# Performance work log

Measured on AMD Instinct MI355X. Metric: run time of the kernel, lower is better.

The kernel has to match this reference:

```python
import jax, jax.numpy as jnp
import numpy as np

SEQ, B, D_IN, D_TRAJ, D_LSTM = 640, 40, 8, 32, 64
NH, DH = 4, 48  # n_head, att_out
EMB = NH * DH  # 192


def setup_inputs() -> dict:
    key = jax.random.key(0)
    ks = jax.random.split(key, 16)
    g = lambda k, shape: (jax.random.normal(k, shape, dtype=jnp.float32) * 0.05)
    z = lambda n: jnp.zeros((n,), jnp.float32)
    return {
        "hist": jax.random.normal(ks[0], (128, 5, 40, D_IN), dtype=jnp.float32),
        "adj": jnp.zeros((B, B), dtype=jnp.int32),  # unused (use_spatial=False)
        "W1": g(ks[1], (D_TRAJ, D_IN)), "b1": z(D_TRAJ),
        "W_ih": g(ks[2], (4 * D_LSTM, D_TRAJ)), "W_hh": g(ks[3], (4 * D_LSTM, D_LSTM)),
        "b_ih": z(4 * D_LSTM), "b_hh": z(4 * D_LSTM),
        "Wq": g(ks[4], (EMB, D_LSTM)), "bq": z(EMB),
        "Wk": g(ks[5], (EMB, D_LSTM)), "bk": z(EMB),
        "Wv": g(ks[6], (EMB, D_LSTM)), "bv": z(EMB),
        "Wa": g(ks[7], (D_LSTM, EMB)), "ba": z(D_LSTM),
        "Wg": g(ks[8], (D_LSTM, EMB)), "bg": z(D_LSTM),
        "gamma": jnp.ones((D_LSTM,), jnp.float32), "beta": z(D_LSTM),
    }


def reference(hist, adj, W1, b1, W_ih, W_hh, b_ih, b_hh,
              Wq, bq, Wk, bk, Wv, bv, Wa, ba, Wg, bg, gamma, beta):
    # trajectory embedding + ELU
    x = jax.nn.elu(jnp.einsum('...f,hf->...h', hist, W1) + b1)
    x = x.reshape(SEQ, B, D_TRAJ)  # hardcoded (128*5, 40, 32) in the module

    # single-layer LSTM (torch gate order i, f, g, o), seq-first
    def step(carry, xt):
        h, c = carry
        gates = xt @ W_ih.T + h @ W_hh.T + b_ih + b_hh
        i, f, g_, o = jnp.split(gates, 4, axis=-1)
        c = jax.nn.sigmoid(f) * c + jax.nn.sigmoid(i) * jnp.tanh(g_)
        h = jax.nn.sigmoid(o) * jnp.tanh(c)
        return (h, c), h

    h0 = jnp.zeros((B, D_LSTM), x.dtype)
    (_, _), seq = jax.lax.scan(step, (h0, h0), x)  # (640, 40, 64)

    # multi-head attention over the 40-agent axis, per time step
    def heads(W, b):
        y = seq @ W.T + b  # (640, 40, 192)
        return y.reshape(SEQ, B, NH, DH).transpose(2, 0, 1, 3)  # (4, 640, 40, 48)

    q, k, v = heads(Wq, bq), heads(Wk, bk), heads(Wv, bv)
    a = jax.nn.softmax(jnp.einsum('hnqd,hnkd->hnqk', q, k) / 8.0, axis=-1)  # /sqrt(64)
    o = jnp.einsum('hnqk,hnkd->hnqd', a, v)  # (4, 640, 40, 48)
    o = o.transpose(1, 2, 0, 3).reshape(SEQ, B, EMB)  # recombine heads -> (640, 40, 192)

    # GLU (dropout rate = 0)
    tv = (o @ Wa.T + ba) * jax.nn.sigmoid(o @ Wg.T + bg)  # (640, 40, 64)

    # Add & LayerNorm (residual with LSTM output)
    y = seq + tv
    mu = y.mean(-1, keepdims=True)
    var = ((y - mu) ** 2).mean(-1, keepdims=True)
    return (y - mu) / jnp.sqrt(var + 1e-5) * gamma + beta
```

## Files before the change

kernel.cpp:

```cpp
#include <hip/hip_runtime.h>

#define SEQ 640
#define BATCH 40
#define D_IN 8
#define D_TRAJ 32
#define D_LSTM 64
#define G4 256
#define NH 4
#define DH 48
#define EMB 192

typedef float v2f __attribute__((ext_vector_type(2)));
typedef float v4f __attribute__((ext_vector_type(4)));
typedef _Float16 h2t __attribute__((ext_vector_type(2)));

__device__ __forceinline__ float sigmoid_f(float x) {
    float e = __expf(-x);
    return __builtin_amdgcn_rcpf(1.f + e);
}
__device__ __forceinline__ float tanh_f(float x) {
    float e = __expf(2.f * x);
    return 1.f - 2.f * __builtin_amdgcn_rcpf(e + 1.f);
}

__global__ void __launch_bounds__(256) k_embed(
    const float* __restrict__ hist, const float* __restrict__ W1,
    const float* __restrict__ b1, const float* __restrict__ W_ih,
    const float* __restrict__ b_ih, const float* __restrict__ b_hh,
    float* __restrict__ gates_x)
{
    __shared__ float sh_hist[BATCH * D_IN];
    __shared__ float sh_traj[BATCH * D_TRAJ];
    const int t = blockIdx.x, tid = threadIdx.x;

    for (int i = tid; i < BATCH * D_IN; i += 256)
        sh_hist[i] = hist[t * BATCH * D_IN + i];
    __syncthreads();

    for (int idx = tid; idx < BATCH * D_TRAJ; idx += 256) {
        int b = idx >> 5, h = idx & 31;
        float acc = b1[h];
        #pragma unroll
        for (int f = 0; f < D_IN; ++f)
            acc += sh_hist[b * D_IN + f] * W1[h * D_IN + f];
        sh_traj[idx] = acc > 0.f ? acc : (__expf(acc) - 1.f);
    }
    __syncthreads();

    float w[D_TRAJ];
    {
        const v4f* wv = (const v4f*)(W_ih + tid * D_TRAJ);
        #pragma unroll
        for (int u = 0; u < 8; ++u) {
            v4f x = wv[u];
            w[4*u] = x.x; w[4*u+1] = x.y; w[4*u+2] = x.z; w[4*u+3] = x.w;
        }
    }
    const float bias = b_ih[tid] + b_hh[tid];
    const int j = tid & 63, g = tid >> 6;

    for (int b = 0; b < BATCH; ++b) {
        float acc = bias;
        #pragma unroll
        for (int h = 0; h < D_TRAJ; ++h)
            acc += sh_traj[b * D_TRAJ + h] * w[h];
        gates_x[((size_t)b * SEQ + t) * G4 + j * 4 + g] = acc;
    }
}

__global__ void __launch_bounds__(64, 1) k_lstm(
    const float* __restrict__ gates_x, const float* __restrict__ W_hh,
    float* __restrict__ seq_out)
{
    const int b = blockIdx.x, j = threadIdx.x;

    h2t wi2[32], wf2[32], wg2[32], wo2[32];
    const float* Wi = W_hh + (0 * 64 + j) * D_LSTM;
    const float* Wf = W_hh + (1 * 64 + j) * D_LSTM;
    const float* Wg = W_hh + (2 * 64 + j) * D_LSTM;
    const float* Wo = W_hh + (3 * 64 + j) * D_LSTM;
    #pragma unroll
    for (int m = 0; m < 32; ++m) {
        wi2[m] = (h2t){(_Float16)Wi[2 * m], (_Float16)Wi[2 * m + 1]};
        wf2[m] = (h2t){(_Float16)Wf[2 * m], (_Float16)Wf[2 * m + 1]};
        wg2[m] = (h2t){(_Float16)Wg[2 * m], (_Float16)Wg[2 * m + 1]};
        wo2[m] = (h2t){(_Float16)Wo[2 * m], (_Float16)Wo[2 * m + 1]};
    }

    const v4f* gxp = (const v4f*)(gates_x + (size_t)b * SEQ * G4);
    v4f g0 = gxp[0 * 64 + j];
    v4f g1 = gxp[1 * 64 + j];
    v4f g2 = gxp[2 * 64 + j];
    v4f g3 = gxp[3 * 64 + j];

    float h = 0.f, c = 0.f;
    float hpf = 0.f;
    const bool odd = (j & 1);

    auto lstm_step = [&](v4f& gk, int t) {
        const int hbits = __builtin_bit_cast(int, hpf);

        float ai0 = gk.x, af0 = gk.y, ag0 = gk.z, ao0 = gk.w;
        float ai1 = 0.f, af1 = 0.f, ag1 = 0.f, ao1 = 0.f;
        #pragma unroll
        for (int m = 0; m < 16; ++m) {
            int pmi = __builtin_amdgcn_readlane(hbits, 2 * m);
            h2t p = __builtin_bit_cast(h2t, pmi);
            ai0 = __builtin_amdgcn_fdot2(wi2[m], p, ai0, false);
            af0 = __builtin_amdgcn_fdot2(wf2[m], p, af0, false);
            ag0 = __builtin_amdgcn_fdot2(wg2[m], p, ag0, false);
            ao0 = __builtin_amdgcn_fdot2(wo2[m], p, ao0, false);
        }
        #pragma unroll
        for (int m = 16; m < 32; ++m) {
            int pmi = __builtin_amdgcn_readlane(hbits, 2 * m);
            h2t p = __builtin_bit_cast(h2t, pmi);
            ai1 = __builtin_amdgcn_fdot2(wi2[m], p, ai1, false);
            af1 = __builtin_amdgcn_fdot2(wf2[m], p, af1, false);
            ag1 = __builtin_amdgcn_fdot2(wg2[m], p, ag1, false);
            ao1 = __builtin_amdgcn_fdot2(wo2[m], p, ao1, false);
        }
        float ai = ai0 + ai1, af = af0 + af1, ag = ag0 + ag1, ao = ao0 + ao1;

        c = sigmoid_f(af) * c + sigmoid_f(ai) * tanh_f(ag);
        h = sigmoid_f(ao) * tanh_f(c);
        seq_out[(size_t)(t * BATCH + b) * D_LSTM + j] = h;

        int own = (int)__builtin_bit_cast(unsigned short, (_Float16)h);
        int nb  = __builtin_amdgcn_update_dpp(0, own, 0xB1, 0xF, 0xF, true);
        int pk  = odd ? (nb | (own << 16)) : (own | (nb << 16));
        hpf = __builtin_bit_cast(float, pk);

        int tp = t + 4; if (tp > SEQ - 1) tp = SEQ - 1;
        gk = gxp[(size_t)tp * 64 + j];
    };

    for (int t = 0; t < SEQ; t += 4) {
        lstm_step(g0, t + 0);
        lstm_step(g1, t + 1);
        lstm_step(g2, t + 2);
        lstm_step(g3, t + 3);
    }
}

#define SAS 68
#define SKVS 152
#define SSS 44
__global__ void __launch_bounds__(256) k_attn(
    const float* __restrict__ seq,
    const float* __restrict__ Wq, const float* __restrict__ bq,
    const float* __restrict__ Wk, const float* __restrict__ bk,
    const float* __restrict__ Wv, const float* __restrict__ bv,
    float* __restrict__ o_buf)
{
    const int h = blockIdx.x, t = blockIdx.y, tid = threadIdx.x;
    __shared__ float sA[BATCH * SAS];
    __shared__ _Float16 skqv[BATCH * SKVS];
    __shared__ float ss[BATCH * SSS];

    for (int i = tid; i < BATCH * D_LSTM; i += 256)
        sA[(i >> 6) * SAS + (i & 63)] = seq[(size_t)t * BATCH * D_LSTM + i];
    __syncthreads();

    if (tid < 144) {
        int m = tid / 48, d = tid - m * 48;
        const float* W = (m == 0) ? Wq : (m == 1) ? Wk : Wv;
        const float* B = (m == 0) ? bq : (m == 1) ? bk : bv;
        const float* wrow = W + (h * DH + d) * D_LSTM;
        float wreg[D_LSTM];
        {
            const v4f* wv = (const v4f*)wrow;
            #pragma unroll
            for (int u = 0; u < 16; ++u) {
                v4f x = wv[u];
                wreg[4*u] = x.x; wreg[4*u+1] = x.y;
                wreg[4*u+2] = x.z; wreg[4*u+3] = x.w;
            }
        }
        const float bias = B[h * DH + d];

        for (int a = 0; a < BATCH; ++a) {
            const v4f* ap = (const v4f*)&sA[a * SAS];
            float acc = bias;
            #pragma unroll
            for (int u = 0; u < 16; ++u) {
                v4f av = ap[u];
                acc += av.x * wreg[4*u]   + av.y * wreg[4*u+1]
                     + av.z * wreg[4*u+2] + av.w * wreg[4*u+3];
            }
            skqv[a * SKVS + tid] = (_Float16)acc;
        }
    }
    __syncthreads();

    for (int idx = tid; idx < BATCH * BATCH; idx += 256) {
        int i = idx / BATCH, jj = idx % BATCH;
        const v4f* qp = (const v4f*)&skqv[i * SKVS];
        const v4f* kp = (const v4f*)&skqv[jj * SKVS + 48];
        float acc = 0.f;
        #pragma unroll
        for (int u = 0; u < 6; ++u) {
            v4f qv = qp[u], kv = kp[u];
            acc = __builtin_amdgcn_fdot2(__builtin_bit_cast(h2t, qv.x),
                    __builtin_bit_cast(h2t, kv.x), acc, false);
            acc = __builtin_amdgcn_fdot2(__builtin_bit_cast(h2t, qv.y),
                    __builtin_bit_cast(h2t, kv.y), acc, false);
            acc = __builtin_amdgcn_fdot2(__builtin_bit_cast(h2t, qv.z),
                    __builtin_bit_cast(h2t, kv.z), acc, false);
            acc = __builtin_amdgcn_fdot2(__builtin_bit_cast(h2t, qv.w),
                    __builtin_bit_cast(h2t, kv.w), acc, false);
        }
        ss[i * SSS + jj] = acc * 0.125f;
    }
    __syncthreads();

    if (tid < BATCH) {
        v4f* rp = (v4f*)&ss[tid * SSS];
        v4f r[10];
        #pragma unroll
        for (int u = 0; u < 10; ++u) r[u] = rp[u];
        float m = -1e30f;
        #pragma unroll
        for (int u = 0; u < 10; ++u)
            m = fmaxf(m, fmaxf(fmaxf(r[u].x, r[u].y), fmaxf(r[u].z, r[u].w)));
        float s = 0.f;
        #pragma unroll
        for (int u = 0; u < 10; ++u) {
            r[u].x = __expf(r[u].x - m); s += r[u].x;
            r[u].y = __expf(r[u].y - m); s += r[u].y;
            r[u].z = __expf(r[u].z - m); s += r[u].z;
            r[u].w = __expf(r[u].w - m); s += r[u].w;
        }
        float inv = __builtin_amdgcn_rcpf(s);
        #pragma unroll
        for (int u = 0; u < 10; ++u) {
            r[u].x *= inv; r[u].y *= inv; r[u].z *= inv; r[u].w *= inv;
            rp[u] = r[u];
        }
    }
    __syncthreads();

    if (tid < 240) {
        int bi = tid / 6, dg = tid % 6, d0 = dg * 8;
        const v4f* sp = (const v4f*)&ss[bi * SSS];
        v4f sr[10];
        #pragma unroll
        for (int u = 0; u < 10; ++u) sr[u] = sp[u];
        float acc[8];
        #pragma unroll
        for (int d = 0; d < 8; ++d) acc[d] = 0.f;
        for (int jj = 0; jj < 40; ++jj) {
            float a = ((const float*)&sr[jj >> 2])[jj & 3];
            v4f vv = *(const v4f*)&skqv[jj * SKVS + 96 + d0];
            #pragma unroll
            for (int w = 0; w < 4; ++w) {
                h2t pr = __builtin_bit_cast(h2t, ((const float*)&vv)[w]);
                acc[2 * w]     += a * (float)pr[0];
                acc[2 * w + 1] += a * (float)pr[1];
            }
        }
        float* ob = &o_buf[((size_t)t * BATCH + bi) * EMB + h * DH + d0];
        *(v4f*)&ob[0] = (v4f){acc[0], acc[1], acc[2], acc[3]};
        *(v4f*)&ob[4] = (v4f){acc[4], acc[5], acc[6], acc[7]};
    }
}

__global__ void __launch_bounds__(256) k_glu_ln(
    const float* __restrict__ seq, const float* __restrict__ obuf,
    const float* __restrict__ Wa, const float* __restrict__ ba,
    const float* __restrict__ Wg, const float* __restrict__ bg,
    const float* __restrict__ gamma, const float* __restrict__ beta,
    float* __restrict__ out)
{
    const int t = blockIdx.x, tid = threadIdx.x;
    __shared__ float so[BATCH * 193];
    __shared__ float sy[BATCH * 65];
    __shared__ float sseq[BATCH * D_LSTM];

    const float* ot = obuf + (size_t)t * BATCH * EMB;
    for (int i = tid; i < BATCH * EMB; i += 256)
        so[(i / EMB) * 193 + (i % EMB)] = ot[i];
    for (int i = tid; i < BATCH * D_LSTM; i += 256)
        sseq[i] = seq[(size_t)t * BATCH * D_LSTM + i];
    __syncthreads();

    const int j = tid >> 2, bgr = tid & 3;
    float acc_a[10], acc_g[10];
    #pragma unroll
    for (int bb = 0; bb < 10; ++bb) { acc_a[bb] = ba[j]; acc_g[bb] = bg[j]; }

    const float* wa = Wa + j * EMB;
    const float* wg = Wg + j * EMB;
    for (int p = 0; p < EMB; ++p) {
        float a = wa[p], g = wg[p];
        #pragma unroll
        for (int bb = 0; bb < 10; ++bb) {
            float o = so[(bgr + 4 * bb) * 193 + p];
            acc_a[bb] += o * a;
            acc_g[bb] += o * g;
        }
    }
    #pragma unroll
    for (int bb = 0; bb < 10; ++bb) {
        int b = bgr + 4 * bb;
        float tv = acc_a[bb] * sigmoid_f(acc_g[bb]);
        sy[b * 65 + j] = sseq[b * D_LSTM + j] + tv;
    }
    __syncthreads();

    const int w = tid >> 6, lane = tid & 63;
    const float gm = gamma[lane], bt = beta[lane];
    for (int rr = 0; rr < 10; ++rr) {
        int b = w + 4 * rr;
        float y = sy[b * 65 + lane];
        float s1 = y, s2 = y * y;
        #pragma unroll
        for (int m = 1; m < 64; m <<= 1) {
            s1 += __shfl_xor(s1, m, 64);
            s2 += __shfl_xor(s2, m, 64);
        }
        float mu  = s1 * (1.f / 64.f);
        float var = s2 * (1.f / 64.f) - mu * mu;
        float inv = rsqrtf(var + 1e-5f);
        out[(size_t)t * BATCH * D_LSTM + b * D_LSTM + lane] =
            (y - mu) * inv * gm + bt;
    }
}

extern "C" void kernel_launch(void* const* d_in, const int* in_sizes, int n_in,
                              void* d_out, int out_size, void* d_ws, size_t ws_size,
                              hipStream_t stream)
{
    const float* hist = (const float*)d_in[0];
    const float* W1   = (const float*)d_in[2];
    const float* b1   = (const float*)d_in[3];
    const float* W_ih = (const float*)d_in[4];
    const float* W_hh = (const float*)d_in[5];
    const float* b_ih = (const float*)d_in[6];
    const float* b_hh = (const float*)d_in[7];
    const float* Wq   = (const float*)d_in[8];
    const float* bq   = (const float*)d_in[9];
    const float* Wk   = (const float*)d_in[10];
    const float* bk   = (const float*)d_in[11];
    const float* Wv   = (const float*)d_in[12];
    const float* bv   = (const float*)d_in[13];
    const float* Wa   = (const float*)d_in[14];
    const float* ba   = (const float*)d_in[15];
    const float* Wg   = (const float*)d_in[16];
    const float* bg   = (const float*)d_in[17];
    const float* gamma = (const float*)d_in[18];
    const float* beta  = (const float*)d_in[19];
    float* out = (float*)d_out;

    float* ws = (float*)d_ws;
    float* gates_x = ws;
    float* seq     = ws + 6553600;
    float* obuf    = ws + 6553600 + 1638400;

    hipLaunchKernelGGL(k_embed, dim3(SEQ), dim3(256), 0, stream,
                       hist, W1, b1, W_ih, b_ih, b_hh, gates_x);
    hipLaunchKernelGGL(k_lstm, dim3(BATCH), dim3(64), 0, stream,
                       gates_x, W_hh, seq);
    hipLaunchKernelGGL(k_attn, dim3(NH, SEQ), dim3(256), 0, stream,
                       seq, Wq, bq, Wk, bk, Wv, bv, obuf);
    hipLaunchKernelGGL(k_glu_ln, dim3(SEQ), dim3(256), 0, stream,
                       seq, obuf, Wa, ba, Wg, bg, gamma, beta, out);
}
```

Baseline: 496.6 us.

## Split LSTM gates across four wavefronts with LDS exchange per step

The recurrent LSTM kernel now uses 256 threads per batch element, one wavefront per gate, so each lane holds one gate row of W_hh and does 32 dot2 ops per step instead of 128. Gate results are exchanged through a double-buffered shared array with a block barrier every time step. The gates_x layout written by the embedding kernel changes to gate-major so each wave reads its own gate contiguously. This shortens the serial dependency chain per step but adds a barrier and LDS round trip to every one of the 640 steps, and all four waves redundantly compute the cell update.

```diff
diff --git a/kernel.cpp b/kernel.cpp
--- a/kernel.cpp
+++ b/kernel.cpp
@@ -64,67 +64,77 @@
         #pragma unroll
         for (int h = 0; h < D_TRAJ; ++h)
             acc += sh_traj[b * D_TRAJ + h] * w[h];
-        gates_x[((size_t)b * SEQ + t) * G4 + j * 4 + g] = acc;
-    }
-}
-
-__global__ void __launch_bounds__(64, 1) k_lstm(
+        gates_x[(((size_t)b * 4 + g) * SEQ + t) * 64 + j] = acc;
+    }
+}
+
+__global__ void __launch_bounds__(256, 1) k_lstm(
     const float* __restrict__ gates_x, const float* __restrict__ W_hh,
     float* __restrict__ seq_out)
 {
-    const int b = blockIdx.x, j = threadIdx.x;
-
-    h2t wi2[32], wf2[32], wg2[32], wo2[32];
-    const float* Wi = W_hh + (0 * 64 + j) * D_LSTM;
-    const float* Wf = W_hh + (1 * 64 + j) * D_LSTM;
-    const float* Wg = W_hh + (2 * 64 + j) * D_LSTM;
-    const float* Wo = W_hh + (3 * 64 + j) * D_LSTM;
-    #pragma unroll
-    for (int m = 0; m < 32; ++m) {
-        wi2[m] = (h2t){(_Float16)Wi[2 * m], (_Float16)Wi[2 * m + 1]};
-        wf2[m] = (h2t){(_Float16)Wf[2 * m], (_Float16)Wf[2 * m + 1]};
-        wg2[m] = (h2t){(_Float16)Wg[2 * m], (_Float16)Wg[2 * m + 1]};
-        wo2[m] = (h2t){(_Float16)Wo[2 * m], (_Float16)Wo[2 * m + 1]};
-    }
-
-    const v4f* gxp = (const v4f*)(gates_x + (size_t)b * SEQ * G4);
-    v4f g0 = gxp[0 * 64 + j];
-    v4f g1 = gxp[1 * 64 + j];
-    v4f g2 = gxp[2 * 64 + j];
-    v4f g3 = gxp[3 * 64 + j];
+    const int b = blockIdx.x;
+    const int tid = threadIdx.x;
+    const int g = tid >> 6;
+    const int j = tid & 63;
+
+    __shared__ float sg[2][4][64];
+
+    h2t w2[32];
+    {
+        const float* Wrow = W_hh + (g * 64 + j) * D_LSTM;
+        #pragma unroll
+        for (int m = 0; m < 32; ++m)
+            w2[m] = (h2t){(_Float16)Wrow[2*m], (_Float16)Wrow[2*m+1]};
+    }
+
+    const float* gx = gates_x + (((size_t)b * 4 + g) * SEQ) * 64 + j;
+    float gq0 = gx[0 * 64];
+    float gq1 = gx[1 * 64];
+    float gq2 = gx[2 * 64];
+    float gq3 = gx[3 * 64];
 
     float h = 0.f, c = 0.f;
     float hpf = 0.f;
     const bool odd = (j & 1);
 
-    auto lstm_step = [&](v4f& gk, int t) {
+    auto step = [&](float& gq, int t) {
         const int hbits = __builtin_bit_cast(int, hpf);
 
-        float ai0 = gk.x, af0 = gk.y, ag0 = gk.z, ao0 = gk.w;
-        float ai1 = 0.f, af1 = 0.f, ag1 = 0.f, ao1 = 0.f;
-        #pragma unroll
-        for (int m = 0; m < 16; ++m) {
-            int pmi = __builtin_amdgcn_readlane(hbits, 2 * m);
-            h2t p = __builtin_bit_cast(h2t, pmi);
-            ai0 = __builtin_amdgcn_fdot2(wi2[m], p, ai0, false);
-            af0 = __builtin_amdgcn_fdot2(wf2[m], p, af0, false);
-            ag0 = __builtin_amdgcn_fdot2(wg2[m], p, ag0, false);
-            ao0 = __builtin_amdgcn_fdot2(wo2[m], p, ao0, false);
-        }
-        #pragma unroll
-        for (int m = 16; m < 32; ++m) {
-            int pmi = __builtin_amdgcn_readlane(hbits, 2 * m);
-            h2t p = __builtin_bit_cast(h2t, pmi);
-            ai1 = __builtin_amdgcn_fdot2(wi2[m], p, ai1, false);
-            af1 = __builtin_amdgcn_fdot2(wf2[m], p, af1, false);
-            ag1 = __builtin_amdgcn_fdot2(wg2[m], p, ag1, false);
-            ao1 = __builtin_amdgcn_fdot2(wo2[m], p, ao1, false);
-        }
-        float ai = ai0 + ai1, af = af0 + af1, ag = ag0 + ag1, ao = ao0 + ao1;
+        float a0 = gq, a1 = 0.f, a2 = 0.f, a3 = 0.f;
+        #pragma unroll
+        for (int m = 0; m < 8; ++m) {
+            h2t p = __builtin_bit_cast(h2t, __builtin_amdgcn_readlane(hbits, 2*m));
+            a0 = __builtin_amdgcn_fdot2(w2[m], p, a0, false);
+        }
+        #pragma unroll
+        for (int m = 8; m < 16; ++m) {
+            h2t p = __builtin_bit_cast(h2t, __builtin_amdgcn_readlane(hbits, 2*m));
+            a1 = __builtin_amdgcn_fdot2(w2[m], p, a1, false);
+        }
+        #pragma unroll
+        for (int m = 16; m < 24; ++m) {
+            h2t p = __builtin_bit_cast(h2t, __builtin_amdgcn_readlane(hbits, 2*m));
+            a2 = __builtin_amdgcn_fdot2(w2[m], p, a2, false);
+        }
+        #pragma unroll
+        for (int m = 24; m < 32; ++m) {
+            h2t p = __builtin_bit_cast(h2t, __builtin_amdgcn_readlane(hbits, 2*m));
+            a3 = __builtin_amdgcn_fdot2(w2[m], p, a3, false);
+        }
+        float a = (a0 + a1) + (a2 + a3);
+
+        const int buf = t & 1;
+        sg[buf][g][j] = a;
+        __syncthreads();
+        float ai = sg[buf][0][j];
+        float af = sg[buf][1][j];
+        float ag = sg[buf][2][j];
+        float ao = sg[buf][3][j];
 
         c = sigmoid_f(af) * c + sigmoid_f(ai) * tanh_f(ag);
         h = sigmoid_f(ao) * tanh_f(c);
-        seq_out[(size_t)(t * BATCH + b) * D_LSTM + j] = h;
+        if (g == 0)
+            seq_out[(size_t)(t * BATCH + b) * D_LSTM + j] = h;
 
         int own = (int)__builtin_bit_cast(unsigned short, (_Float16)h);
         int nb  = __builtin_amdgcn_update_dpp(0, own, 0xB1, 0xF, 0xF, true);
@@ -132,14 +142,14 @@
         hpf = __builtin_bit_cast(float, pk);
 
         int tp = t + 4; if (tp > SEQ - 1) tp = SEQ - 1;
-        gk = gxp[(size_t)tp * 64 + j];
+        gq = gx[(size_t)tp * 64];
     };
 
     for (int t = 0; t < SEQ; t += 4) {
-        lstm_step(g0, t + 0);
-        lstm_step(g1, t + 1);
-        lstm_step(g2, t + 2);
-        lstm_step(g3, t + 3);
+        step(gq0, t + 0);
+        step(gq1, t + 1);
+        step(gq2, t + 2);
+        step(gq3, t + 3);
     }
 }
 
@@ -359,7 +369,7 @@
 
     hipLaunchKernelGGL(k_embed, dim3(SEQ), dim3(256), 0, stream,
                        hist, W1, b1, W_ih, b_ih, b_hh, gates_x);
-    hipLaunchKernelGGL(k_lstm, dim3(BATCH), dim3(64), 0, stream,
+    hipLaunchKernelGGL(k_lstm, dim3(BATCH), dim3(256), 0, stream,
                        gates_x, W_hh, seq);
     hipLaunchKernelGGL(k_attn, dim3(NH, SEQ), dim3(256), 0, stream,
                        seq, Wq, bq, Wk, bk, Wv, bv, obuf);
```

Measured after the change: 467.8 us. -5.8%, faster.
